# Kernel optimization log

Measured on AMD Instinct MI355X. Metric: run time of the kernel, lower is better.

Reference implementation:

```python
import jax, jax.numpy as jnp
import numpy as np

INPUT_DIM = 1024
HIDDEN_DIM = 1024
BATCH = 8
SEQ = 2048


def setup_inputs() -> dict:
    key = jax.random.key(0)
    ks = jax.random.split(key, 7)
    s = 1.0 / np.sqrt(INPUT_DIM)
    return {
        "subgraph_embeddings": jax.random.normal(ks[0], (BATCH, SEQ, INPUT_DIM), dtype=jnp.float32),
        "Wq": jax.random.uniform(ks[1], (INPUT_DIM, HIDDEN_DIM), jnp.float32, -s, s),
        "bq": jax.random.uniform(ks[2], (HIDDEN_DIM,), jnp.float32, -s, s),
        "Wk": jax.random.uniform(ks[3], (INPUT_DIM, HIDDEN_DIM), jnp.float32, -s, s),
        "bk": jax.random.uniform(ks[4], (HIDDEN_DIM,), jnp.float32, -s, s),
        "Wv": jax.random.uniform(ks[5], (INPUT_DIM, HIDDEN_DIM), jnp.float32, -s, s),
        "bv": jax.random.uniform(ks[6], (HIDDEN_DIM,), jnp.float32, -s, s),
    }


def reference(subgraph_embeddings, Wq, bq, Wk, bk, Wv, bv):
    x = subgraph_embeddings  # [B, S, D]
    Q = jnp.einsum('bsd,dh->bsh', x, Wq) + bq
    K = jnp.einsum('bsd,dh->bsh', x, Wk) + bk
    V = jnp.einsum('bsd,dh->bsh', x, Wv) + bv
    scale = jnp.sqrt(jnp.float32(HIDDEN_DIM))
    scores = jnp.einsum('bqh,bkh->bqk', Q, K) / scale  # [B, S, S]
    weights = jax.nn.softmax(scores, axis=-1)
    return jnp.einsum('bqk,bkh->bqh', weights, V)
```

## Files before the change

kernel.cpp:

```cpp
#include <hip/hip_runtime.h>
#include <hip/hip_bf16.h>
#include <stdint.h>

typedef unsigned short u16;
typedef unsigned int u32;
typedef __attribute__((ext_vector_type(8))) short bf16x8;
typedef __attribute__((ext_vector_type(4))) float f32x4;

#define S_LEN 2048
#define D_DIM 1024
#define H_DIM 1024
#define BATCH 8
#define M_TOTAL (BATCH * S_LEN)

__device__ __forceinline__ u16 f2b(float f) {
  u32 u = __builtin_bit_cast(u32, f);
  u32 r = (u + 0x7fffu + ((u >> 16) & 1u)) >> 16;
  return (u16)r;
}

__global__ __launch_bounds__(256) void cast_x_kernel(const float* __restrict__ in,
                                                     u16* __restrict__ out, int n8) {
  int i = blockIdx.x * 256 + threadIdx.x;
  if (i >= n8) return;
  const float4* p = (const float4*)in;
  float4 a = p[2 * i], b = p[2 * i + 1];
  u32 w0 = (u32)f2b(a.x) | ((u32)f2b(a.y) << 16);
  u32 w1 = (u32)f2b(a.z) | ((u32)f2b(a.w) << 16);
  u32 w2 = (u32)f2b(b.x) | ((u32)f2b(b.y) << 16);
  u32 w3 = (u32)f2b(b.z) | ((u32)f2b(b.w) << 16);
  ((uint4*)out)[i] = make_uint4(w0, w1, w2, w3);
}

__global__ __launch_bounds__(256) void wcast_all_kernel(
    const float* __restrict__ Wq, const float* __restrict__ Wk,
    const float* __restrict__ Wv, const float* __restrict__ bq,
    const float* __restrict__ bk, u16* __restrict__ Wtqk,
    u16* __restrict__ Wtv, float* __restrict__ bqk, float* __restrict__ lsum) {
  __shared__ float tile[32][33];
  int z = blockIdx.z;
  const float* W = (z == 0) ? Wq : (z == 1) ? Wk : Wv;
  u16* Wt = (z == 0) ? Wtqk : (z == 1) ? (Wtqk + 1024 * 1024) : Wtv;
  int h0 = blockIdx.x * 32, d0 = blockIdx.y * 32;
  int tx = threadIdx.x & 31, ty = threadIdx.x >> 5;
#pragma unroll
  for (int r = ty; r < 32; r += 8)
    tile[r][tx] = W[(size_t)(d0 + r) * H_DIM + h0 + tx];
  if (blockIdx.x == 0 && blockIdx.y == 0) {
    if (z == 0) {
      for (int i = threadIdx.x; i < 1024; i += 256) bqk[i] = bq[i];
    } else if (z == 1) {
      for (int i = threadIdx.x; i < 1024; i += 256) bqk[1024 + i] = bk[i];
    } else {
      for (int i = threadIdx.x; i < M_TOTAL; i += 256) lsum[i] = 0.f;
    }
  }
  __syncthreads();
#pragma unroll
  for (int r = ty; r < 32; r += 8)
    Wt[(size_t)(h0 + r) * D_DIM + d0 + tx] = f2b(tile[tx][r]);
}

template <int BIAS, int EPI, bool OUT_BF16>
__global__ __launch_bounds__(512, 2) void gemm256(
    const u16* __restrict__ A, const u16* __restrict__ Bt, void* __restrict__ Cout,
    const float* __restrict__ bias, float* __restrict__ lsum,
    int M, int N, int K, int lda, int ldb, int ldc,
    long long aBatch, long long bBatch, long long cBatch, float scale) {
  __shared__ __align__(16) u16 As[2][256 * 64];
  __shared__ __align__(16) u16 Bs[2][256 * 64];
  const int tid = threadIdx.x;
  const int wave = tid >> 6, lane = tid & 63;
  const int quad = lane >> 4, lr = lane & 15;
  const int wm = (wave >> 2) * 128, wn = (wave & 3) * 64;
  const int row0 = blockIdx.x * 256, col0 = blockIdx.y * 256;
  A += (size_t)blockIdx.z * (size_t)aBatch;
  Bt += (size_t)blockIdx.z * (size_t)bBatch;

  f32x4 acc[8][4] = {};

  auto AsL = (__attribute__((address_space(3))) char*)&As[0][0];
  auto BsL = (__attribute__((address_space(3))) char*)&Bs[0][0];
  const char* Ab = (const char*)A;
  const char* Bb = (const char*)Bt;

  auto stage_aq = [&](int buf, int q, int k0) {
#pragma unroll
    for (int rr = 0; rr < 2; ++rr) {
      int idx = rr * 512 + tid;
      int i = idx >> 3, ch = idx & 7;
      int row = ((i >> 6) << 7) | (q << 6) | (i & 63);
      int cs = ch ^ (row & 7);
      const void* g = Ab + (((size_t)(row0 + row) * lda + (size_t)(k0 + cs * 8)) * 2);
      __builtin_amdgcn_global_load_lds(
          (const __attribute__((address_space(1))) void*)g,
          (__attribute__((address_space(3))) void*)(AsL + (size_t)buf * 32768 +
                                                   (size_t)(row * 8 + ch) * 16),
          16, 0, 0);
    }
  };
  auto stage_bq = [&](int buf, int q, int k0) {
#pragma unroll
    for (int rr = 0; rr < 2; ++rr) {
      int idx = rr * 512 + tid;
      int i = idx >> 3, ch = idx & 7;
      int row = ((i >> 5) << 6) | (q << 5) | (i & 31);
      int cs = ch ^ (row & 7);
      const void* g = Bb + (((size_t)(col0 + row) * ldb + (size_t)(k0 + cs * 8)) * 2);
      __builtin_amdgcn_global_load_lds(
          (const __attribute__((address_space(1))) void*)g,
          (__attribute__((address_space(3))) void*)(BsL + (size_t)buf * 32768 +
                                                   (size_t)(row * 8 + ch) * 16),
          16, 0, 0);
    }
  };

#define READ_A(MH)                                                              \
  _Pragma("unroll") for (int ksi = 0; ksi < 2; ++ksi)                           \
  _Pragma("unroll") for (int i = 0; i < 4; ++i) {                               \
    int r = wm + ((MH) * 4 + i) * 16 + lr;                                      \
    int cc = (ksi * 4 + quad) ^ (r & 7);                                        \
    afr[ksi][i] = *(const bf16x8*)&As[cur][r * 64 + cc * 8];                    \
  }
#define READ_B(NH)                                                              \
  _Pragma("unroll") for (int ksi = 0; ksi < 2; ++ksi)                           \
  _Pragma("unroll") for (int j = 0; j < 2; ++j) {                               \
    int r = wn + ((NH) * 2 + j) * 16 + lr;                                      \
    int cc = (ksi * 4 + quad) ^ (r & 7);                                        \
    bfr[NH][j][ksi] = *(const bf16x8*)&Bs[cur][r * 64 + cc * 8];                \
  }
#define MFMA_QUAD(MH, NH)                                                       \
  _Pragma("unroll") for (int ksi = 0; ksi < 2; ++ksi)                           \
  _Pragma("unroll") for (int i = 0; i < 4; ++i)                                 \
  _Pragma("unroll") for (int j = 0; j < 2; ++j)                                 \
    acc[(MH) * 4 + i][(NH) * 2 + j] = __builtin_amdgcn_mfma_f32_16x16x32_bf16(  \
        afr[ksi][i], bfr[NH][j][ksi], acc[(MH) * 4 + i][(NH) * 2 + j], 0, 0, 0);

#define BAR()                                              \
  __builtin_amdgcn_s_barrier();                            \
  __builtin_amdgcn_sched_barrier(0)

  const int nkt = K >> 6;

  stage_aq(0, 0, 0); stage_bq(0, 0, 0); stage_bq(0, 1, 0); stage_aq(0, 1, 0);
  stage_aq(1, 0, 64); stage_bq(1, 0, 64); stage_bq(1, 1, 64); stage_aq(1, 1, 64);
  asm volatile("s_waitcnt vmcnt(8)" ::: "memory");
  __builtin_amdgcn_sched_barrier(0);
  BAR();

  bf16x8 afr[2][4];
  bf16x8 bfr[2][2][2];

  for (int t = 0; t <= nkt - 3; ++t) {
    const int cur = t & 1;
    const int kn = (t + 2) << 6;
    READ_A(0);
    READ_B(0);
    __builtin_amdgcn_s_setprio(1);
    MFMA_QUAD(0, 0);
    __builtin_amdgcn_s_setprio(0);
    BAR();
    READ_B(1);
    stage_aq(cur, 0, kn);
    stage_bq(cur, 0, kn);
    __builtin_amdgcn_s_setprio(1);
    MFMA_QUAD(0, 1);
    __builtin_amdgcn_s_setprio(0);
    BAR();
    READ_A(1);
    stage_bq(cur, 1, kn);
    __builtin_amdgcn_s_setprio(1);
    MFMA_QUAD(1, 0);
    __builtin_amdgcn_s_setprio(0);
    BAR();
    stage_aq(cur, 1, kn);
    __builtin_amdgcn_s_setprio(1);
    MFMA_QUAD(1, 1);
    __builtin_amdgcn_s_setprio(0);
    asm volatile("s_waitcnt vmcnt(8)" ::: "memory");
    __builtin_amdgcn_sched_barrier(0);
    BAR();
  }
  {
    const int cur = (nkt - 2) & 1;
    READ_A(0);
    READ_B(0);
    MFMA_QUAD(0, 0);
    READ_B(1);
    MFMA_QUAD(0, 1);
    READ_A(1);
    MFMA_QUAD(1, 0);
    MFMA_QUAD(1, 1);
    asm volatile("s_waitcnt vmcnt(0)" ::: "memory");
    __builtin_amdgcn_sched_barrier(0);
    BAR();
  }
  {
    const int cur = (nkt - 1) & 1;
    READ_A(0);
    READ_B(0);
    MFMA_QUAD(0, 0);
    READ_B(1);
    MFMA_QUAD(0, 1);
    READ_A(1);
    MFMA_QUAD(1, 0);
    MFMA_QUAD(1, 1);
  }
#undef READ_A
#undef READ_B
#undef MFMA_QUAD
#undef BAR

  const long long lrow0 = (long long)blockIdx.z * M + row0;

  if constexpr (EPI == 1) {
    u16* C = (u16*)Cout + (size_t)blockIdx.z * (size_t)cBatch;
#pragma unroll
    for (int i = 0; i < 8; ++i) {
#pragma unroll
      for (int ii = 0; ii < 4; ++ii) {
        int r = wm + i * 16 + quad * 4 + ii;
        float rowsum = 0.f;
#pragma unroll
        for (int j = 0; j < 4; ++j) {
          float e = __expf(acc[i][j][ii] * scale);
          rowsum += e;
          C[(size_t)(row0 + r) * ldc + (col0 + wn + j * 16 + lr)] = f2b(e);
        }
#pragma unroll
        for (int off = 1; off < 16; off <<= 1) rowsum += __shfl_xor(rowsum, off);
        if (lr == 0) atomicAdd(lsum + lrow0 + r, rowsum);
      }
    }
    return;
  }

#pragma unroll
  for (int i = 0; i < 8; ++i) {
#pragma unroll
    for (int ii = 0; ii < 4; ++ii) {
      int r = wm + i * 16 + quad * 4 + ii;
      float radd = 0.f, rmul = 1.f;
      if (BIAS == 2) radd = bias[row0 + r];
      if (EPI == 2) rmul = 1.0f / lsum[lrow0 + r];
#pragma unroll
      for (int j = 0; j < 4; ++j) {
        int c = col0 + wn + j * 16 + lr;
        float v = acc[i][j][ii] * rmul + radd;
        if (BIAS == 1) v += bias[c];
        if constexpr (OUT_BF16) {
          u16* C = (u16*)Cout + (size_t)blockIdx.z * (size_t)cBatch;
          C[(size_t)(row0 + r) * ldc + c] = f2b(v);
        } else {
          float* C = (float*)Cout + (size_t)blockIdx.z * (size_t)cBatch;
          C[(size_t)(row0 + r) * ldc + c] = v;
        }
      }
    }
  }
}

extern "C" void kernel_launch(void* const* d_in, const int* in_sizes, int n_in,
                              void* d_out, int out_size, void* d_ws, size_t ws_size,
                              hipStream_t stream) {
  const float* x = (const float*)d_in[0];
  const float* Wq = (const float*)d_in[1];
  const float* bq = (const float*)d_in[2];
  const float* Wk = (const float*)d_in[3];
  const float* bk = (const float*)d_in[4];
  const float* Wv = (const float*)d_in[5];
  const float* bv = (const float*)d_in[6];
  float* out = (float*)d_out;

  char* ws = (char*)d_ws;
  u16* xb = (u16*)ws;   ws += (size_t)M_TOTAL * D_DIM * 2;
  u16* Wtqk = (u16*)ws; ws += (size_t)2 * H_DIM * D_DIM * 2;
  u16* Wtv = (u16*)ws;  ws += (size_t)H_DIM * D_DIM * 2;
  u16* QKm = (u16*)ws;  ws += (size_t)M_TOTAL * 2 * H_DIM * 2;
  u16* Vt = (u16*)ws;   ws += (size_t)BATCH * H_DIM * S_LEN * 2;
  u16* Sm = (u16*)ws;   ws += (size_t)BATCH * S_LEN * S_LEN * 2;
  float* bqk = (float*)ws;  ws += 2048 * 4;
  float* lsum = (float*)ws; ws += (size_t)M_TOTAL * 4;

  cast_x_kernel<<<(M_TOTAL * D_DIM / 8 + 255) / 256, 256, 0, stream>>>(
      x, xb, M_TOTAL * D_DIM / 8);
  wcast_all_kernel<<<dim3(32, 32, 3), 256, 0, stream>>>(
      Wq, Wk, Wv, bq, bk, Wtqk, Wtv, bqk, lsum);

  gemm256<1, 0, true><<<dim3(64, 8, 1), 512, 0, stream>>>(
      xb, Wtqk, QKm, bqk, nullptr, M_TOTAL, 2 * H_DIM, D_DIM,
      D_DIM, D_DIM, 2 * H_DIM, 0, 0, 0, 0.f);

  gemm256<2, 0, true><<<dim3(4, 8, BATCH), 512, 0, stream>>>(
      Wtv, xb, Vt, bv, nullptr, H_DIM, S_LEN, D_DIM,
      D_DIM, D_DIM, S_LEN,
      0LL, (long long)S_LEN * D_DIM, (long long)H_DIM * S_LEN, 0.f);

  gemm256<0, 1, true><<<dim3(8, 8, BATCH), 512, 0, stream>>>(
      QKm, QKm + H_DIM, Sm, nullptr, lsum, S_LEN, S_LEN, H_DIM,
      2 * H_DIM, 2 * H_DIM, S_LEN,
      (long long)S_LEN * 2 * H_DIM, (long long)S_LEN * 2 * H_DIM,
      (long long)S_LEN * S_LEN, 0.03125f);

  gemm256<0, 2, false><<<dim3(8, 4, BATCH), 512, 0, stream>>>(
      Sm, Vt, out, nullptr, lsum, S_LEN, H_DIM, S_LEN,
      S_LEN, S_LEN, H_DIM,
      (long long)S_LEN * S_LEN, (long long)H_DIM * S_LEN,
      (long long)S_LEN * H_DIM, 0.f);
}
```

Before: 401.3 us.

## Restructure GEMM main loop to an 8-wave ping-pong schedule with explicit LDS waits

Reworks the K-loop schedule so each MFMA quadrant follows an LDS read, a global-to-LDS stage, a barrier and an explicit lgkmcnt wait. The last A quarter of the next tile is now issued one iteration later, so the prologue and loop use vmcnt(6) instead of vmcnt(8). The aim is to interleave global loads, LDS reads and MFMA more evenly across waves, in the style of hipBLASLt ping-pong kernels. It adds more barriers per iteration, and the split of the stage across iterations has to stay correct with the double-buffer indices.

```diff
diff --git a/kernel.cpp b/kernel.cpp
--- a/kernel.cpp
+++ b/kernel.cpp
@@ -136,15 +136,18 @@
     acc[(MH) * 4 + i][(NH) * 2 + j] = __builtin_amdgcn_mfma_f32_16x16x32_bf16(  \
         afr[ksi][i], bfr[NH][j][ksi], acc[(MH) * 4 + i][(NH) * 2 + j], 0, 0, 0);
 
-#define BAR()                                              \
-  __builtin_amdgcn_s_barrier();                            \
+#define BAR() __builtin_amdgcn_s_barrier()
+#define WAIT_LGKM0()                                       \
+  asm volatile("s_waitcnt lgkmcnt(0)" ::: "memory");       \
   __builtin_amdgcn_sched_barrier(0)
+#define PRIO1() __builtin_amdgcn_s_setprio(1)
+#define PRIO0() __builtin_amdgcn_s_setprio(0)
 
   const int nkt = K >> 6;
 
   stage_aq(0, 0, 0); stage_bq(0, 0, 0); stage_bq(0, 1, 0); stage_aq(0, 1, 0);
-  stage_aq(1, 0, 64); stage_bq(1, 0, 64); stage_bq(1, 1, 64); stage_aq(1, 1, 64);
-  asm volatile("s_waitcnt vmcnt(8)" ::: "memory");
+  stage_aq(1, 0, 64); stage_bq(1, 0, 64); stage_bq(1, 1, 64);
+  asm volatile("s_waitcnt vmcnt(6)" ::: "memory");
   __builtin_amdgcn_sched_barrier(0);
   BAR();
 
@@ -152,45 +155,58 @@
   bf16x8 bfr[2][2][2];
 
   for (int t = 0; t <= nkt - 3; ++t) {
-    const int cur = t & 1;
-    const int kn = (t + 2) << 6;
+    const int cur = t & 1, nxt = cur ^ 1;
+    const int kn1 = (t + 1) << 6, kn2 = (t + 2) << 6;
     READ_A(0);
     READ_B(0);
-    __builtin_amdgcn_s_setprio(1);
-    MFMA_QUAD(0, 0);
-    __builtin_amdgcn_s_setprio(0);
+    stage_aq(nxt, 1, kn1);
+    asm volatile("s_waitcnt lgkmcnt(8)" ::: "memory");
+    BAR();
+    WAIT_LGKM0();
+    PRIO1(); MFMA_QUAD(0, 0); PRIO0();
     BAR();
     READ_B(1);
-    stage_aq(cur, 0, kn);
-    stage_bq(cur, 0, kn);
-    __builtin_amdgcn_s_setprio(1);
-    MFMA_QUAD(0, 1);
-    __builtin_amdgcn_s_setprio(0);
+    stage_aq(cur, 0, kn2);
+    BAR();
+    WAIT_LGKM0();
+    PRIO1(); MFMA_QUAD(0, 1); PRIO0();
     BAR();
     READ_A(1);
-    stage_bq(cur, 1, kn);
-    __builtin_amdgcn_s_setprio(1);
-    MFMA_QUAD(1, 0);
-    __builtin_amdgcn_s_setprio(0);
-    BAR();
-    stage_aq(cur, 1, kn);
-    __builtin_amdgcn_s_setprio(1);
-    MFMA_QUAD(1, 1);
-    __builtin_amdgcn_s_setprio(0);
-    asm volatile("s_waitcnt vmcnt(8)" ::: "memory");
+    stage_bq(cur, 0, kn2);
+    BAR();
+    WAIT_LGKM0();
+    PRIO1(); MFMA_QUAD(1, 0); PRIO0();
+    BAR();
+    stage_bq(cur, 1, kn2);
+    BAR();
+    PRIO1(); MFMA_QUAD(1, 1); PRIO0();
+    asm volatile("s_waitcnt vmcnt(6)" ::: "memory");
     __builtin_amdgcn_sched_barrier(0);
     BAR();
   }
   {
-    const int cur = (nkt - 2) & 1;
+    const int t = nkt - 2;
+    const int cur = t & 1, nxt = cur ^ 1;
+    const int kn1 = (t + 1) << 6;
     READ_A(0);
     READ_B(0);
-    MFMA_QUAD(0, 0);
+    stage_aq(nxt, 1, kn1);
+    asm volatile("s_waitcnt lgkmcnt(8)" ::: "memory");
+    BAR();
+    WAIT_LGKM0();
+    PRIO1(); MFMA_QUAD(0, 0); PRIO0();
+    BAR();
     READ_B(1);
-    MFMA_QUAD(0, 1);
+    BAR();
+    WAIT_LGKM0();
+    PRIO1(); MFMA_QUAD(0, 1); PRIO0();
+    BAR();
     READ_A(1);
-    MFMA_QUAD(1, 0);
-    MFMA_QUAD(1, 1);
+    BAR();
+    WAIT_LGKM0();
+    PRIO1(); MFMA_QUAD(1, 0); PRIO0();
+    BAR();
+    PRIO1(); MFMA_QUAD(1, 1); PRIO0();
     asm volatile("s_waitcnt vmcnt(0)" ::: "memory");
     __builtin_amdgcn_sched_barrier(0);
     BAR();
@@ -210,6 +226,9 @@
 #undef READ_B
 #undef MFMA_QUAD
 #undef BAR
+#undef WAIT_LGKM0
+#undef PRIO1
+#undef PRIO0
 
   const long long lrow0 = (long long)blockIdx.z * M + row0;
 
```

Result: no change. 396.3 us (-1.2%).
